# Optimization experiments

Measured on AMD Instinct MI355X. Metric: run time of the kernel, lower is better.

The kernel has to match this reference:

```python
import jax, jax.numpy as jnp
import numpy as np

N = 50000      # nodes
E = 160000     # edges
NFEAT = 1024
NHID = 512
NCLASS = 64


def _unif(k, shape, fan):
    s = 1.0 / np.sqrt(fan)
    return jax.random.uniform(k, shape, jnp.float32, -s, s)


def setup_inputs() -> dict:
    key = jax.random.key(0)
    ks = jax.random.split(key, 16)
    x = jax.random.normal(ks[0], (N, NFEAT), jnp.float32)
    adj_row = jax.random.randint(ks[1], (E,), 0, N, jnp.int32)
    adj_col = jax.random.randint(ks[2], (E,), 0, N, jnp.int32)
    adj_val = jax.random.uniform(ks[3], (E,), jnp.float32)
    # gc1: nfeat -> nhid (stdv = 1/sqrt(out_features))
    W1 = _unif(ks[4], (NFEAT, NHID), NHID)
    b1 = _unif(ks[5], (NHID,), NHID)
    # residual projection for gc1 (nn.Linear nfeat->nhid)
    p1W = _unif(ks[6], (NFEAT, NHID), NFEAT)
    p1b = _unif(ks[7], (NHID,), NFEAT)
    # gc3: nhid -> nhid (shared across 4 applications)
    W3 = _unif(ks[8], (NHID, NHID), NHID)
    b3 = _unif(ks[9], (NHID,), NHID)
    # gc2: nhid -> nclass
    W2 = _unif(ks[10], (NHID, NCLASS), NCLASS)
    b2 = _unif(ks[11], (NCLASS,), NCLASS)
    # residual projection for gc2 (nn.Linear nhid->nclass)
    p2W = _unif(ks[12], (NHID, NCLASS), NHID)
    p2b = _unif(ks[13], (NCLASS,), NHID)
    return {"x": x, "adj_row": adj_row, "adj_col": adj_col, "adj_val": adj_val,
            "W1": W1, "b1": b1, "p1W": p1W, "p1b": p1b,
            "W3": W3, "b3": b3, "W2": W2, "b2": b2, "p2W": p2W, "p2b": p2b}


def _spmm(row, col, val, support):
    # out[i] = sum_e val[e] * support[col[e]] for row[e] == i   (adj @ support)
    return jax.ops.segment_sum(val[:, None] * support[col], row, num_segments=N)


def reference(x, adj_row, adj_col, adj_val, W1, b1, p1W, p1b, W3, b3, W2, b2, p2W, p2b):
    def gc_proj(inp, W, b, pW, pb):
        # shapes differ -> projected residual
        out = _spmm(adj_row, adj_col, adj_val, inp @ W) + b
        return jax.nn.relu(out + inp @ pW + pb)

    def gc_res(inp, W, b):
        # same shape -> identity residual
        out = _spmm(adj_row, adj_col, adj_val, inp @ W) + b
        return jax.nn.relu(out + inp)

    h = jax.nn.relu(gc_proj(x, W1, b1, p1W, p1b))       # [N, NHID]
    for _ in range(4):                                   # gc3 shared weights x4
        h = jax.nn.relu(gc_res(h, W3, b3))
    h = gc_proj(h, W2, b2, p2W, p2b)                     # [N, NCLASS]
    return jax.nn.log_softmax(h, axis=1)
```

## Files before the change

### kernel.cpp

```cpp
#include <hip/hip_runtime.h>

typedef __attribute__((ext_vector_type(8))) short bf16x8;
typedef __attribute__((ext_vector_type(8))) unsigned short ushort8;
typedef __attribute__((ext_vector_type(4))) float f32x4;

#define NNODES 50000
#define NEDGES 160000
#define MP     50048
#define NB_SCAN 196

__device__ __forceinline__ float bf2f(unsigned short u) {
  return __uint_as_float(((unsigned int)u) << 16);
}
__device__ __forceinline__ unsigned short f2bf(float f) {
  unsigned int u = __float_as_uint(f);
  u += 0x7fffu + ((u >> 16) & 1u);
  return (unsigned short)(u >> 16);
}
__device__ __forceinline__ void gld16(const void* g, void* l) {
  __builtin_amdgcn_global_load_lds((__attribute__((address_space(1))) void*)g,
                                   (__attribute__((address_space(3))) void*)l, 16, 0, 0);
}

__global__ void k_hist(const int* __restrict__ row, int* __restrict__ cnt, int n) {
  int i = blockIdx.x * 256 + threadIdx.x;
  if (i < n) atomicAdd(&cnt[row[i]], 1);
}

__global__ void k_block_reduce(const int* __restrict__ cnt, int* __restrict__ bsum, int n) {
  __shared__ int sd[256];
  int i = blockIdx.x * 256 + threadIdx.x;
  sd[threadIdx.x] = (i < n) ? cnt[i] : 0;
  __syncthreads();
  for (int o = 128; o > 0; o >>= 1) {
    if (threadIdx.x < o) sd[threadIdx.x] += sd[threadIdx.x + o];
    __syncthreads();
  }
  if (threadIdx.x == 0) bsum[blockIdx.x] = sd[0];
}

__global__ void k_scan_bsum(const int* __restrict__ bsum, int* __restrict__ boff, int nb,
                            int* __restrict__ rowptr, int n, int E) {
  __shared__ int sd[256];
  int v = (threadIdx.x < nb) ? bsum[threadIdx.x] : 0;
  sd[threadIdx.x] = v;
  __syncthreads();
  for (int o = 1; o < 256; o <<= 1) {
    int t = (threadIdx.x >= o) ? sd[threadIdx.x - o] : 0;
    __syncthreads();
    sd[threadIdx.x] += t;
    __syncthreads();
  }
  if (threadIdx.x < nb) boff[threadIdx.x] = sd[threadIdx.x] - v;
  if (threadIdx.x == 0) rowptr[n] = E;
}

__global__ void k_block_scan(const int* __restrict__ cnt, const int* __restrict__ boff,
                             int* __restrict__ rowptr, int* __restrict__ cursor, int n) {
  __shared__ int sd[256];
  int i = blockIdx.x * 256 + threadIdx.x;
  int v = (i < n) ? cnt[i] : 0;
  sd[threadIdx.x] = v;
  __syncthreads();
  for (int o = 1; o < 256; o <<= 1) {
    int t = (threadIdx.x >= o) ? sd[threadIdx.x - o] : 0;
    __syncthreads();
    sd[threadIdx.x] += t;
    __syncthreads();
  }
  if (i < n) {
    int r = boff[blockIdx.x] + sd[threadIdx.x] - v;
    rowptr[i] = r;
    cursor[i] = r;
  }
}

__global__ void k_scatter(const int* __restrict__ row, const int* __restrict__ col,
                          const float* __restrict__ val, int* __restrict__ cursor,
                          int* __restrict__ scol, float* __restrict__ sval, int n) {
  int e = blockIdx.x * 256 + threadIdx.x;
  if (e < n) {
    int p = atomicAdd(&cursor[row[e]], 1);
    scol[p] = col[e];
    sval[p] = val[e];
  }
}

__global__ void k_cast_x(const float* __restrict__ x, unsigned short* __restrict__ xb, int nRealRows) {
  size_t idx = ((size_t)blockIdx.x * 256 + threadIdx.x) * 8;
  if (idx >= (size_t)MP * 1024) return;
  int row = (int)(idx >> 10);
  ushort8 o;
  if (row < nRealRows) {
    float4 a = *(const float4*)(x + idx);
    float4 b = *(const float4*)(x + idx + 4);
    o[0] = f2bf(a.x); o[1] = f2bf(a.y); o[2] = f2bf(a.z); o[3] = f2bf(a.w);
    o[4] = f2bf(b.x); o[5] = f2bf(b.y); o[6] = f2bf(b.z); o[7] = f2bf(b.w);
  } else {
    o = (ushort8){0,0,0,0,0,0,0,0};
  }
  *(ushort8*)(xb + idx) = o;
}

__global__ void k_packT(const float* __restrict__ src, int K, int srcW, int nc,
                        unsigned short* __restrict__ dst, int dstOff) {
  __shared__ float tile[32][33];
  int k0 = blockIdx.x * 32, n0 = blockIdx.y * 32;
  int tx = threadIdx.x, ty = threadIdx.y;
  for (int i = ty; i < 32; i += 8)
    tile[i][tx] = src[(size_t)(k0 + i) * srcW + (n0 + tx)];
  __syncthreads();
  for (int i = ty; i < 32; i += 8)
    dst[(size_t)(dstOff + n0 + i) * K + (k0 + tx)] = f2bf(tile[tx][i]);
}

__global__ void k_pack_bias(const float* __restrict__ b1, const float* __restrict__ p1b,
                            const float* __restrict__ b2, const float* __restrict__ p2b,
                            float* __restrict__ bias1, float* __restrict__ bias2) {
  int t = threadIdx.x;
  bias1[t] = b1[t] + p1b[t];
  if (t < 64) bias2[t] = b2[t] + p2b[t];
}

__global__ __launch_bounds__(256) void k_gemm_bt(
    const unsigned short* __restrict__ A, const unsigned short* __restrict__ Bt,
    unsigned short* __restrict__ C, int M, int N, int K) {
  __shared__ __align__(16) unsigned short As[128 * 32];
  __shared__ __align__(16) unsigned short Bs[128 * 32];
  const int ntc = N >> 7;
  const int mt = blockIdx.x / ntc;
  const int nt = blockIdx.x % ntc;
  const int t = threadIdx.x;
  const int w = t >> 6, lane = t & 63;
  const int wr = w >> 1, wc = w & 1;
  f32x4 acc[4][4] = {};
  const unsigned short* ga = A + (size_t)(mt * 128 + (t >> 2)) * K + (t & 3) * 8;
  const unsigned short* gb = Bt + (size_t)(nt * 128 + (t >> 2)) * K + (t & 3) * 8;
  unsigned short* lA = &As[w * 512];
  unsigned short* lB = &Bs[w * 512];
  const size_t rowskip = (size_t)64 * K;
  for (int kt = 0; kt < K; kt += 32) {
    gld16(ga + kt, lA);
    gld16(ga + kt + rowskip, lA + 2048);
    gld16(gb + kt, lB);
    gld16(gb + kt + rowskip, lB + 2048);
    __syncthreads();
    bf16x8 af[4], bfr[4];
#pragma unroll
    for (int m = 0; m < 4; ++m)
      af[m] = *(const bf16x8*)&As[(wr * 64 + m * 16 + (lane & 15)) * 32 + (lane >> 4) * 8];
#pragma unroll
    for (int n = 0; n < 4; ++n)
      bfr[n] = *(const bf16x8*)&Bs[(wc * 64 + n * 16 + (lane & 15)) * 32 + (lane >> 4) * 8];
#pragma unroll
    for (int m = 0; m < 4; ++m)
#pragma unroll
      for (int n = 0; n < 4; ++n)
        acc[m][n] = __builtin_amdgcn_mfma_f32_16x16x32_bf16(af[m], bfr[n], acc[m][n], 0, 0, 0);
    __syncthreads();
  }
  const int r0 = mt * 128 + wr * 64 + (lane >> 4) * 4;
  const int c0 = nt * 128 + wc * 64 + (lane & 15);
#pragma unroll
  for (int m = 0; m < 4; ++m)
#pragma unroll
    for (int n = 0; n < 4; ++n)
#pragma unroll
      for (int r = 0; r < 4; ++r)
        C[(size_t)(r0 + m * 16 + r) * N + (c0 + n * 16)] = f2bf(acc[m][n][r]);
}

__global__ __launch_bounds__(256) void k_spmm_ep512(
    const int* __restrict__ rowptr, const int* __restrict__ scol, const float* __restrict__ sval,
    const unsigned short* __restrict__ s, int sStride,
    const unsigned short* __restrict__ res, int resStride,
    const float* __restrict__ bias,
    unsigned short* __restrict__ o, int oStride, int nReal, int nTot) {
  int gw = (blockIdx.x * 256 + threadIdx.x) >> 6;
  int lane = threadIdx.x & 63;
  if (gw >= nTot) return;
  unsigned short* op = o + (size_t)gw * oStride + lane * 8;
  if (gw >= nReal) {
    *(ushort8*)op = (ushort8){0,0,0,0,0,0,0,0};
    return;
  }
  float acc[8] = {0.f,0.f,0.f,0.f,0.f,0.f,0.f,0.f};
  int e0 = rowptr[gw], e1 = rowptr[gw + 1];
  for (int e = e0; e < e1; ++e) {
    int c = scol[e];
    float v = sval[e];
    ushort8 svv = *(const ushort8*)(s + (size_t)c * sStride + lane * 8);
#pragma unroll
    for (int k = 0; k < 8; ++k) acc[k] += v * bf2f(svv[k]);
  }
  ushort8 rv = *(const ushort8*)(res + (size_t)gw * resStride + lane * 8);
  ushort8 ov;
#pragma unroll
  for (int k = 0; k < 8; ++k) {
    float tt = acc[k] + bias[lane * 8 + k] + bf2f(rv[k]);
    ov[k] = f2bf(fmaxf(tt, 0.f));
  }
  *(ushort8*)op = ov;
}

__global__ __launch_bounds__(256) void k_spmm_lsm(
    const int* __restrict__ rowptr, const int* __restrict__ scol, const float* __restrict__ sval,
    const unsigned short* __restrict__ g2, const float* __restrict__ bias2,
    float* __restrict__ out, int n) {
  int gw = (blockIdx.x * 256 + threadIdx.x) >> 6;
  int lane = threadIdx.x & 63;
  if (gw >= n) return;
  int e0 = rowptr[gw], e1 = rowptr[gw + 1];
  float acc = 0.f;
  for (int e = e0; e < e1; ++e) {
    int c = scol[e];
    acc += sval[e] * bf2f(g2[(size_t)c * 128 + lane]);
  }
  float t = acc + bias2[lane] + bf2f(g2[(size_t)gw * 128 + 64 + lane]);
  float v = fmaxf(t, 0.f);
  float m = v;
#pragma unroll
  for (int o = 32; o > 0; o >>= 1) m = fmaxf(m, __shfl_xor(m, o));
  float ex = __expf(v - m);
  float ss = ex;
#pragma unroll
  for (int o = 32; o > 0; o >>= 1) ss += __shfl_xor(ss, o);
  out[(size_t)gw * 64 + lane] = v - m - __logf(ss);
}

extern "C" void kernel_launch(void* const* d_in, const int* in_sizes, int n_in,
                              void* d_out, int out_size, void* d_ws, size_t ws_size,
                              hipStream_t stream) {
  const float* x    = (const float*)d_in[0];
  const int*   arow = (const int*)d_in[1];
  const int*   acol = (const int*)d_in[2];
  const float* aval = (const float*)d_in[3];
  const float* W1   = (const float*)d_in[4];
  const float* b1   = (const float*)d_in[5];
  const float* p1W  = (const float*)d_in[6];
  const float* p1b  = (const float*)d_in[7];
  const float* W3   = (const float*)d_in[8];
  const float* b3   = (const float*)d_in[9];
  const float* W2   = (const float*)d_in[10];
  const float* b2   = (const float*)d_in[11];
  const float* p2W  = (const float*)d_in[12];
  const float* p2b  = (const float*)d_in[13];
  float* out = (float*)d_out;

  char* wsp = (char*)d_ws;
  size_t off = 0;
  auto take = [&](size_t bytes) -> char* {
    char* p = wsp + off;
    off = (off + bytes + 255) & ~(size_t)255;
    return p;
  };
  unsigned short* xb  = (unsigned short*)take((size_t)MP * 1024 * 2);
  unsigned short* g1  = (unsigned short*)take((size_t)MP * 1024 * 2);
  unsigned short* B1t = (unsigned short*)take((size_t)1024 * 1024 * 2);
  unsigned short* W3t = (unsigned short*)take((size_t)512 * 512 * 2);
  unsigned short* B2t = (unsigned short*)take((size_t)128 * 512 * 2);
  float* bias1 = (float*)take(512 * 4);
  float* bias2 = (float*)take(64 * 4);
  int*   cnt    = (int*)take((size_t)NNODES * 4);
  int*   rowptr = (int*)take((size_t)(NNODES + 1) * 4);
  int*   bsum   = (int*)take(256 * 4);
  int*   boff   = (int*)take(256 * 4);
  int*   scol   = (int*)take((size_t)NEDGES * 4);
  float* sval   = (float*)take((size_t)NEDGES * 4);
  unsigned short* h  = xb;
  unsigned short* s  = g1;
  unsigned short* g2 = g1;

  hipMemsetAsync(cnt, 0, (size_t)NNODES * 4, stream);
  k_hist<<<(NEDGES + 255) / 256, 256, 0, stream>>>(arow, cnt, NEDGES);
  k_block_reduce<<<NB_SCAN, 256, 0, stream>>>(cnt, bsum, NNODES);
  k_scan_bsum<<<1, 256, 0, stream>>>(bsum, boff, NB_SCAN, rowptr, NNODES, NEDGES);
  k_block_scan<<<NB_SCAN, 256, 0, stream>>>(cnt, boff, rowptr, cnt, NNODES);
  k_scatter<<<(NEDGES + 255) / 256, 256, 0, stream>>>(arow, acol, aval, cnt, scol, sval, NEDGES);

  k_cast_x<<<(int)(((size_t)MP * 1024 / 8 + 255) / 256), 256, 0, stream>>>(x, xb, NNODES);
  k_packT<<<dim3(1024 / 32, 512 / 32), dim3(32, 8), 0, stream>>>(W1, 1024, 512, 512, B1t, 0);
  k_packT<<<dim3(1024 / 32, 512 / 32), dim3(32, 8), 0, stream>>>(p1W, 1024, 512, 512, B1t, 512);
  k_packT<<<dim3(512 / 32, 512 / 32), dim3(32, 8), 0, stream>>>(W3, 512, 512, 512, W3t, 0);
  k_packT<<<dim3(512 / 32, 64 / 32), dim3(32, 8), 0, stream>>>(W2, 512, 64, 64, B2t, 0);
  k_packT<<<dim3(512 / 32, 64 / 32), dim3(32, 8), 0, stream>>>(p2W, 512, 64, 64, B2t, 64);
  k_pack_bias<<<1, 512, 0, stream>>>(b1, p1b, b2, p2b, bias1, bias2);

  k_gemm_bt<<<391 * 8, 256, 0, stream>>>(xb, B1t, g1, MP, 1024, 1024);
  k_spmm_ep512<<<MP / 4, 256, 0, stream>>>(rowptr, scol, sval, g1, 1024, g1 + 512, 1024,
                                           bias1, h, 512, NNODES, MP);
  for (int i = 0; i < 4; ++i) {
    k_gemm_bt<<<391 * 4, 256, 0, stream>>>(h, W3t, s, MP, 512, 512);
    k_spmm_ep512<<<MP / 4, 256, 0, stream>>>(rowptr, scol, sval, s, 512, h, 512,
                                             b3, h, 512, NNODES, MP);
  }
  k_gemm_bt<<<391, 256, 0, stream>>>(h, B2t, g2, MP, 128, 512);
  k_spmm_lsm<<<(NNODES + 3) / 4, 256, 0, stream>>>(rowptr, scol, sval, g2, bias2, out, NNODES);
}
```

Baseline: 699.0 us.

## Add 256x256-tile double-buffered bf16 GEMM with XCD swizzle for large projections

Adds a new GEMM kernel using 256x256 output tiles, 512 threads and 128KB of LDS double-buffering. It uses direct global-to-LDS loads with XOR-swizzled chunks and interleaves MFMA phases with the next tile's staging. Workgroups are remapped so consecutive tiles land on the same XCD, and the row padding is raised to a multiple of 256 to fit the new tile. The goal is more operand reuse and better overlap in the 1024- and 512-wide GEMMs, at the cost of lower occupancy, more padded rows and heavy register use.

```diff
diff --git a/kernel.cpp b/kernel.cpp
--- a/kernel.cpp
+++ b/kernel.cpp
@@ -6,7 +6,7 @@
 
 #define NNODES 50000
 #define NEDGES 160000
-#define MP     50048
+#define MP     50176
 #define NB_SCAN 196
 
 __device__ __forceinline__ float bf2f(unsigned short u) {
@@ -120,6 +120,126 @@
   int t = threadIdx.x;
   bias1[t] = b1[t] + p1b[t];
   if (t < 64) bias2[t] = b2[t] + p2b[t];
+}
+
+__global__ __launch_bounds__(512, 2) void k_gemm256(
+    const unsigned short* __restrict__ A, const unsigned short* __restrict__ Bt,
+    unsigned short* __restrict__ C, int M, int N, int K) {
+  extern __shared__ char smem[];
+  const int NT = N >> 8;
+  const int nwg = gridDim.x;
+  const int q = nwg >> 3, r = nwg & 7;
+  const int xcd = blockIdx.x & 7, local = blockIdx.x >> 3;
+  const int swz = (xcd < r ? xcd * (q + 1) : r * (q + 1) + (xcd - r) * q) + local;
+  const int mt = swz / NT, nt = swz % NT;
+
+  const int tid = threadIdx.x;
+  const int w = tid >> 6, lane = tid & 63;
+  const int wr = w >> 2, wc = w & 3;
+
+  const int srow = tid >> 3;
+  const int schunk = (tid & 7) ^ (srow & 7);
+  const unsigned short* gA = A + (size_t)(mt * 256 + srow) * K + schunk * 8;
+  const unsigned short* gB = Bt + (size_t)(nt * 256 + srow) * K + schunk * 8;
+  const size_t rs64 = (size_t)64 * K;
+
+  const int l15 = lane & 15;
+  const int cs0 = (((lane >> 4)) ^ (lane & 7)) << 4;
+  const int cs1 = (((lane >> 4) | 4) ^ (lane & 7)) << 4;
+  const int aBase0 = (wr * 128 + l15) * 128 + cs0;
+  const int aBase1 = (wr * 128 + l15) * 128 + cs1;
+  const int bBase0 = 32768 + (wc * 64 + l15) * 128 + cs0;
+  const int bBase1 = 32768 + (wc * 64 + l15) * 128 + cs1;
+
+  f32x4 acc[8][4] = {};
+  bf16x8 af[4][2], bfr[2][2];
+  const int ktiles = K >> 6;
+
+#define LDSV(off) (*(const bf16x8*)(smem + (off)))
+#define STAGE_A(buf, kn) { char* db = smem + (buf) + (w << 10); \
+    const unsigned short* g = gA + (kn); \
+    gld16(g, db); gld16(g + rs64, db + 8192); \
+    gld16(g + 2 * rs64, db + 16384); gld16(g + 3 * rs64, db + 24576); }
+#define STAGE_B(buf, kn) { char* db = smem + (buf) + 32768 + (w << 10); \
+    const unsigned short* g = gB + (kn); \
+    gld16(g, db); gld16(g + rs64, db + 8192); \
+    gld16(g + 2 * rs64, db + 16384); gld16(g + 3 * rs64, db + 24576); }
+#define MFMA16(MOFF, NOFF) \
+  __builtin_amdgcn_s_setprio(1); \
+  _Pragma("unroll") \
+  for (int m = 0; m < 4; ++m) \
+    _Pragma("unroll") \
+    for (int n = 0; n < 2; ++n) { \
+      acc[(MOFF) + m][(NOFF) + n] = __builtin_amdgcn_mfma_f32_16x16x32_bf16( \
+          af[m][0], bfr[n][0], acc[(MOFF) + m][(NOFF) + n], 0, 0, 0); \
+      acc[(MOFF) + m][(NOFF) + n] = __builtin_amdgcn_mfma_f32_16x16x32_bf16( \
+          af[m][1], bfr[n][1], acc[(MOFF) + m][(NOFF) + n], 0, 0, 0); \
+    } \
+  __builtin_amdgcn_s_setprio(0);
+
+  STAGE_A(0, 0)
+  STAGE_B(0, 0)
+  __syncthreads();
+
+  for (int t = 0; t < ktiles; ++t) {
+    const int cur = (t & 1) << 16;
+    const int nxt = cur ^ 65536;
+    const int kn = (t + 1) << 6;
+    const bool more = (t + 1) < ktiles;
+#pragma unroll
+    for (int m = 0; m < 4; ++m) {
+      af[m][0] = LDSV(cur + aBase0 + m * 2048);
+      af[m][1] = LDSV(cur + aBase1 + m * 2048);
+    }
+#pragma unroll
+    for (int n = 0; n < 2; ++n) {
+      bfr[n][0] = LDSV(cur + bBase0 + n * 2048);
+      bfr[n][1] = LDSV(cur + bBase1 + n * 2048);
+    }
+    if (more) STAGE_A(nxt, kn)
+    __builtin_amdgcn_s_barrier();
+    MFMA16(0, 0)
+    __builtin_amdgcn_s_barrier();
+#pragma unroll
+    for (int n = 0; n < 2; ++n) {
+      bfr[n][0] = LDSV(cur + bBase0 + (n + 2) * 2048);
+      bfr[n][1] = LDSV(cur + bBase1 + (n + 2) * 2048);
+    }
+    if (more) STAGE_B(nxt, kn)
+    __builtin_amdgcn_s_barrier();
+    MFMA16(0, 2)
+    __builtin_amdgcn_s_barrier();
+#pragma unroll
+    for (int m = 0; m < 4; ++m) {
+      af[m][0] = LDSV(cur + aBase0 + (m + 4) * 2048);
+      af[m][1] = LDSV(cur + aBase1 + (m + 4) * 2048);
+    }
+    __builtin_amdgcn_s_barrier();
+    MFMA16(4, 2)
+    __builtin_amdgcn_s_barrier();
+#pragma unroll
+    for (int n = 0; n < 2; ++n) {
+      bfr[n][0] = LDSV(cur + bBase0 + n * 2048);
+      bfr[n][1] = LDSV(cur + bBase1 + n * 2048);
+    }
+    __builtin_amdgcn_s_barrier();
+    MFMA16(4, 0)
+    __syncthreads();
+  }
+
+  const int r0 = mt * 256 + wr * 128 + (lane >> 4) * 4;
+  const int c0 = nt * 256 + wc * 64 + (lane & 15);
+#pragma unroll
+  for (int m = 0; m < 8; ++m)
+#pragma unroll
+    for (int n = 0; n < 4; ++n)
+#pragma unroll
+      for (int j = 0; j < 4; ++j)
+        C[(size_t)(r0 + m * 16 + j) * N + (c0 + n * 16)] = f2bf(acc[m][n][j]);
+#undef LDSV
+#undef STAGE_A
+#undef STAGE_B
+#undef MFMA16
 }
 
 __global__ __launch_bounds__(256) void k_gemm_bt(
@@ -286,14 +406,14 @@
   k_packT<<<dim3(512 / 32, 64 / 32), dim3(32, 8), 0, stream>>>(p2W, 512, 64, 64, B2t, 64);
   k_pack_bias<<<1, 512, 0, stream>>>(b1, p1b, b2, p2b, bias1, bias2);
 
-  k_gemm_bt<<<391 * 8, 256, 0, stream>>>(xb, B1t, g1, MP, 1024, 1024);
+  k_gemm256<<<196 * 4, 512, 131072, stream>>>(xb, B1t, g1, MP, 1024, 1024);
   k_spmm_ep512<<<MP / 4, 256, 0, stream>>>(rowptr, scol, sval, g1, 1024, g1 + 512, 1024,
                                            bias1, h, 512, NNODES, MP);
   for (int i = 0; i < 4; ++i) {
-    k_gemm_bt<<<391 * 4, 256, 0, stream>>>(h, W3t, s, MP, 512, 512);
+    k_gemm256<<<196 * 2, 512, 131072, stream>>>(h, W3t, s, MP, 512, 512);
     k_spmm_ep512<<<MP / 4, 256, 0, stream>>>(rowptr, scol, sval, s, 512, h, 512,
                                              b3, h, 512, NNODES, MP);
   }
-  k_gemm_bt<<<391, 256, 0, stream>>>(h, B2t, g2, MP, 128, 512);
+  k_gemm_bt<<<MP / 128, 256, 0, stream>>>(h, B2t, g2, MP, 128, 512);
   k_spmm_lsm<<<(NNODES + 3) / 4, 256, 0, stream>>>(rowptr, scol, sval, g2, bias2, out, NNODES);
 }
```

After: 639.1 us. -8.6%, faster.

## Add 256x256-tile GEMM with 4-stage LDS pipeline and XCD-aware block swizzle

Applied to the files above, without the earlier changes.

Adds a new 512-thread GEMM kernel that computes 256x256 output tiles. It stages K-slices through a 4-deep ring of direct global-to-LDS buffers with XOR-swizzled chunks and explicit waitcnt/barrier scheduling, and raises wave priority around the MFMA clusters. Blocks are remapped across the 8 XCDs so neighbouring tiles share cache. It replaces the 128x128 GEMM for the wide layers, and the row padding grows to a multiple of 256. This trades occupancy (one 128KB-LDS block per CU) for higher data reuse and overlap, and it pads the work with extra rows.

```diff
diff --git a/kernel.cpp b/kernel.cpp
--- a/kernel.cpp
+++ b/kernel.cpp
@@ -6,7 +6,7 @@
 
 #define NNODES 50000
 #define NEDGES 160000
-#define MP     50048
+#define MP     50176
 #define NB_SCAN 196
 
 __device__ __forceinline__ float bf2f(unsigned short u) {
@@ -120,6 +120,102 @@
   int t = threadIdx.x;
   bias1[t] = b1[t] + p1b[t];
   if (t < 64) bias2[t] = b2[t] + p2b[t];
+}
+
+
+__device__ __forceinline__ void rd4(bf16x8 (&f)[4], const char* smem, int off) {
+#pragma unroll
+  for (int i = 0; i < 4; ++i) f[i] = *(const bf16x8*)(smem + off + i * 1024);
+}
+
+__device__ __forceinline__ void cluster(f32x4 (&acc)[4][4], const bf16x8 (&a)[4], const bf16x8 (&b)[4]) {
+#pragma unroll
+  for (int m = 0; m < 4; ++m)
+#pragma unroll
+    for (int n = 0; n < 4; ++n)
+      acc[m][n] = __builtin_amdgcn_mfma_f32_16x16x32_bf16(a[m], b[n], acc[m][n], 0, 0, 0);
+}
+
+__global__ __launch_bounds__(512, 1) void k_gemm256(
+    const unsigned short* __restrict__ A, const unsigned short* __restrict__ Bt,
+    unsigned short* __restrict__ C, int M, int N, int K) {
+  extern __shared__ char smem[];
+  const int NT = N >> 8;
+  const int nwg = gridDim.x;
+  const int q = nwg >> 3, r = nwg & 7;
+  const int xcd = blockIdx.x & 7, local = blockIdx.x >> 3;
+  const int swz = (xcd < r ? xcd * (q + 1) : r * (q + 1) + (xcd - r) * q) + local;
+  const int mt = swz / NT, nt = swz % NT;
+
+  const int tid = threadIdx.x;
+  const int w = tid >> 6, lane = tid & 63;
+  const int wr = w >> 2, wc = w & 3;
+
+  const int srow = tid >> 2, c0 = tid & 3;
+  const int schunk = c0 ^ ((srow >> 1) & 3);
+  const unsigned short* gA = A + (size_t)(mt * 256 + srow) * K + schunk * 8;
+  const unsigned short* gB = Bt + (size_t)(nt * 256 + srow) * K + schunk * 8;
+  const size_t rs = (size_t)128 * K;
+  const int wb = w << 10;
+
+  const int l15 = lane & 15;
+  const int cpos = ((lane >> 4) ^ ((l15 >> 1) & 3)) << 4;
+  const int aOff = (wr * 128 + l15) * 64 + cpos;
+  const int bOff = 16384 + (wc * 64 + l15) * 64 + cpos;
+
+  f32x4 accLo[4][4] = {}, accHi[4][4] = {};
+  const int T = K >> 5;
+
+  auto STAGE = [&](int t) {
+    char* base = smem + ((t & 3) << 15);
+    const unsigned short* a = gA + t * 32;
+    const unsigned short* b = gB + t * 32;
+    gld16(a, base + wb);
+    gld16(a + rs, base + 8192 + wb);
+    gld16(b, base + 16384 + wb);
+    gld16(b + rs, base + 24576 + wb);
+  };
+
+#define KITER(T_, WSTR, DOSTAGE) { \
+    const int bb = ((T_) & 3) << 15; \
+    asm volatile("s_waitcnt vmcnt(" WSTR ")" ::: "memory"); \
+    __builtin_amdgcn_sched_barrier(0); \
+    __builtin_amdgcn_s_barrier(); \
+    __builtin_amdgcn_sched_barrier(0); \
+    bf16x8 af[4], bfr[4]; \
+    rd4(af, smem, bb + aOff); \
+    rd4(bfr, smem, bb + bOff); \
+    if (DOSTAGE) STAGE((T_) + 3); \
+    __builtin_amdgcn_s_barrier(); \
+    __builtin_amdgcn_s_setprio(1); \
+    cluster(accLo, af, bfr); \
+    __builtin_amdgcn_s_setprio(0); \
+    __builtin_amdgcn_s_barrier(); \
+    rd4(af, smem, bb + aOff + 4096); \
+    __builtin_amdgcn_s_setprio(1); \
+    cluster(accHi, af, bfr); \
+    __builtin_amdgcn_s_setprio(0); \
+    __builtin_amdgcn_sched_barrier(0); \
+  }
+
+  STAGE(0); STAGE(1); STAGE(2);
+  for (int t = 0; t < T - 3; ++t) KITER(t, "8", true)
+  KITER(T - 3, "8", false)
+  KITER(T - 2, "4", false)
+  KITER(T - 1, "0", false)
+#undef KITER
+
+  const int r0 = mt * 256 + wr * 128 + (lane >> 4) * 4;
+  const int c0e = nt * 256 + wc * 64 + l15;
+#pragma unroll
+  for (int m = 0; m < 4; ++m)
+#pragma unroll
+    for (int n = 0; n < 4; ++n)
+#pragma unroll
+      for (int j = 0; j < 4; ++j) {
+        C[(size_t)(r0 + m * 16 + j) * N + (c0e + n * 16)] = f2bf(accLo[m][n][j]);
+        C[(size_t)(r0 + 64 + m * 16 + j) * N + (c0e + n * 16)] = f2bf(accHi[m][n][j]);
+      }
 }
 
 __global__ __launch_bounds__(256) void k_gemm_bt(
@@ -286,14 +382,14 @@
   k_packT<<<dim3(512 / 32, 64 / 32), dim3(32, 8), 0, stream>>>(p2W, 512, 64, 64, B2t, 64);
   k_pack_bias<<<1, 512, 0, stream>>>(b1, p1b, b2, p2b, bias1, bias2);
 
-  k_gemm_bt<<<391 * 8, 256, 0, stream>>>(xb, B1t, g1, MP, 1024, 1024);
+  k_gemm256<<<196 * 4, 512, 131072, stream>>>(xb, B1t, g1, MP, 1024, 1024);
   k_spmm_ep512<<<MP / 4, 256, 0, stream>>>(rowptr, scol, sval, g1, 1024, g1 + 512, 1024,
                                            bias1, h, 512, NNODES, MP);
   for (int i = 0; i < 4; ++i) {
-    k_gemm_bt<<<391 * 4, 256, 0, stream>>>(h, W3t, s, MP, 512, 512);
+    k_gemm256<<<196 * 2, 512, 131072, stream>>>(h, W3t, s, MP, 512, 512);
     k_spmm_ep512<<<MP / 4, 256, 0, stream>>>(rowptr, scol, sval, s, 512, h, 512,
                                              b3, h, 512, NNODES, MP);
   }
-  k_gemm_bt<<<391, 256, 0, stream>>>(h, B2t, g2, MP, 128, 512);
+  k_gemm_bt<<<MP / 128, 256, 0, stream>>>(h, B2t, g2, MP, 128, 512);
   k_spmm_lsm<<<(NNODES + 3) / 4, 256, 0, stream>>>(rowptr, scol, sval, g2, bias2, out, NNODES);
 }
```

New measurement: 646.2 us. 7.6% less time.

## Add 256x256-tile triple-buffered bf16 MFMA GEMM with XCD swizzle for wide layers

Applied to the files above, without the earlier changes.

Adds a new GEMM kernel for the 1024-wide and 512-wide layers. It uses 256x256 output tiles with 512 threads, a three-stage LDS ring fed by global_load_lds, XOR-swizzled LDS chunks, staged loads interleaved with MFMA groups under s_setprio, and block-index remapping across the 8 XCDs. The row padding MP is raised to a multiple of 256 so the larger tiles fit. The larger tiles are meant to cut global and LDS traffic per FLOP and improve L2 locality, at the cost of 96 KB of LDS and one workgroup per CU.

```diff
diff --git a/kernel.cpp b/kernel.cpp
--- a/kernel.cpp
+++ b/kernel.cpp
@@ -6,7 +6,7 @@
 
 #define NNODES 50000
 #define NEDGES 160000
-#define MP     50048
+#define MP     50176
 #define NB_SCAN 196
 
 __device__ __forceinline__ float bf2f(unsigned short u) {
@@ -120,6 +120,107 @@
   int t = threadIdx.x;
   bias1[t] = b1[t] + p1b[t];
   if (t < 64) bias2[t] = b2[t] + p2b[t];
+}
+
+
+__device__ __forceinline__ void mfma8(f32x4* accA, f32x4* accB,
+                                      bf16x8 a0, bf16x8 a1, const bf16x8* bfr) {
+#pragma unroll
+  for (int n = 0; n < 4; ++n)
+    accA[n] = __builtin_amdgcn_mfma_f32_16x16x32_bf16(a0, bfr[n], accA[n], 0, 0, 0);
+#pragma unroll
+  for (int n = 0; n < 4; ++n)
+    accB[n] = __builtin_amdgcn_mfma_f32_16x16x32_bf16(a1, bfr[n], accB[n], 0, 0, 0);
+}
+
+__global__ __launch_bounds__(512, 1) void k_gemm256(
+    const unsigned short* __restrict__ A, const unsigned short* __restrict__ Bt,
+    unsigned short* __restrict__ C, int M, int N, int K) {
+  extern __shared__ char smem[];
+  const int NT = N >> 8;
+  const int nwg = gridDim.x;
+  const int q = nwg >> 3, r = nwg & 7;
+  const int xcd = blockIdx.x & 7, local = blockIdx.x >> 3;
+  const int swz = (xcd < r ? xcd * (q + 1) : r * (q + 1) + (xcd - r) * q) + local;
+  const int mt = swz / NT, nt = swz % NT;
+
+  const int tid = threadIdx.x;
+  const int w = tid >> 6, lane = tid & 63;
+  const int wr = w >> 2, wc = w & 3;
+
+  const int srow = w * 16 + (lane >> 2);
+  const int schunk = (lane & 3) ^ ((lane >> 3) & 3);
+  const unsigned short* gA = A + (size_t)(mt * 256 + srow) * K + schunk * 8;
+  const unsigned short* gB = Bt + (size_t)(nt * 256 + srow) * K + schunk * 8;
+  const size_t rs128 = (size_t)128 * K;
+  const int wb = w << 10;
+
+  const int l15 = lane & 15;
+  const int cpos = ((lane >> 4) ^ ((l15 >> 1) & 3)) << 4;
+  const int aOff = (wr * 128 + l15) * 64 + cpos;
+  const int bOff = 16384 + (wc * 64 + l15) * 64 + cpos;
+
+  f32x4 acc[8][4] = {};
+  const int T = K >> 5;
+
+  auto stage_u = [&](int t, int u) {
+    char* dst = smem + (t % 3) * 32768 + u * 8192 + wb;
+    const unsigned short* g = (u < 2 ? gA : gB) + ((u & 1) ? rs128 : 0) + (size_t)t * 32;
+    gld16(g, dst);
+  };
+
+#pragma unroll
+  for (int u = 0; u < 4; ++u) stage_u(0, u);
+#pragma unroll
+  for (int u = 0; u < 4; ++u) stage_u(1, u);
+
+  for (int t = 0; t < T; ++t) {
+    const int bb = (t % 3) * 32768;
+    if (t < T - 1) asm volatile("s_waitcnt vmcnt(4)" ::: "memory");
+    else           asm volatile("s_waitcnt vmcnt(0)" ::: "memory");
+    __builtin_amdgcn_s_barrier();
+    const bool st = t < T - 2;
+    bf16x8 bfr[4], a0, a1;
+#pragma unroll
+    for (int n = 0; n < 4; ++n) bfr[n] = *(const bf16x8*)(smem + bb + bOff + n * 1024);
+    a0 = *(const bf16x8*)(smem + bb + aOff);
+    a1 = *(const bf16x8*)(smem + bb + aOff + 1024);
+    if (st) stage_u(t + 2, 0);
+    __builtin_amdgcn_s_setprio(1);
+    mfma8(acc[0], acc[1], a0, a1, bfr);
+    __builtin_amdgcn_s_setprio(0);
+    __builtin_amdgcn_s_barrier();
+    a0 = *(const bf16x8*)(smem + bb + aOff + 2 * 1024);
+    a1 = *(const bf16x8*)(smem + bb + aOff + 3 * 1024);
+    if (st) stage_u(t + 2, 1);
+    __builtin_amdgcn_s_setprio(1);
+    mfma8(acc[2], acc[3], a0, a1, bfr);
+    __builtin_amdgcn_s_setprio(0);
+    __builtin_amdgcn_s_barrier();
+    a0 = *(const bf16x8*)(smem + bb + aOff + 4 * 1024);
+    a1 = *(const bf16x8*)(smem + bb + aOff + 5 * 1024);
+    if (st) stage_u(t + 2, 2);
+    __builtin_amdgcn_s_setprio(1);
+    mfma8(acc[4], acc[5], a0, a1, bfr);
+    __builtin_amdgcn_s_setprio(0);
+    __builtin_amdgcn_s_barrier();
+    a0 = *(const bf16x8*)(smem + bb + aOff + 6 * 1024);
+    a1 = *(const bf16x8*)(smem + bb + aOff + 7 * 1024);
+    if (st) stage_u(t + 2, 3);
+    __builtin_amdgcn_s_setprio(1);
+    mfma8(acc[6], acc[7], a0, a1, bfr);
+    __builtin_amdgcn_s_setprio(0);
+  }
+
+  const int r0 = mt * 256 + wr * 128 + (lane >> 4) * 4;
+  const int c0e = nt * 256 + wc * 64 + l15;
+#pragma unroll
+  for (int m = 0; m < 8; ++m)
+#pragma unroll
+    for (int n = 0; n < 4; ++n)
+#pragma unroll
+      for (int j = 0; j < 4; ++j)
+        C[(size_t)(r0 + m * 16 + j) * N + (c0e + n * 16)] = f2bf(acc[m][n][j]);
 }
 
 __global__ __launch_bounds__(256) void k_gemm_bt(
@@ -286,14 +387,14 @@
   k_packT<<<dim3(512 / 32, 64 / 32), dim3(32, 8), 0, stream>>>(p2W, 512, 64, 64, B2t, 64);
   k_pack_bias<<<1, 512, 0, stream>>>(b1, p1b, b2, p2b, bias1, bias2);
 
-  k_gemm_bt<<<391 * 8, 256, 0, stream>>>(xb, B1t, g1, MP, 1024, 1024);
+  k_gemm256<<<196 * 4, 512, 98304, stream>>>(xb, B1t, g1, MP, 1024, 1024);
   k_spmm_ep512<<<MP / 4, 256, 0, stream>>>(rowptr, scol, sval, g1, 1024, g1 + 512, 1024,
                                            bias1, h, 512, NNODES, MP);
   for (int i = 0; i < 4; ++i) {
-    k_gemm_bt<<<391 * 4, 256, 0, stream>>>(h, W3t, s, MP, 512, 512);
+    k_gemm256<<<196 * 2, 512, 98304, stream>>>(h, W3t, s, MP, 512, 512);
     k_spmm_ep512<<<MP / 4, 256, 0, stream>>>(rowptr, scol, sval, s, 512, h, 512,
                                              b3, h, 512, NNODES, MP);
   }
-  k_gemm_bt<<<391, 256, 0, stream>>>(h, B2t, g2, MP, 128, 512);
+  k_gemm_bt<<<MP / 128, 256, 0, stream>>>(h, B2t, g2, MP, 128, 512);
   k_spmm_lsm<<<(NNODES + 3) / 4, 256, 0, stream>>>(rowptr, scol, sval, g2, bias2, out, NNODES);
 }
```

New measurement: 630.5 us. 9.8% less time.
